# Kernel tuning notes

Hardware: AMD Instinct MI355X
Metric: run time of the kernel (lower is better)

## Reference

```python
import math
import jax, jax.numpy as jnp
import numpy as np

B, T, C, HS = 4, 4096, 1024, 64  # batch, seq, n_embd, head_size=n_embd//n_head

def setup_inputs() -> dict:
    key = jax.random.key(0)
    k0, k1, k2, k3 = jax.random.split(key, 4)
    x = jax.random.normal(k0, (B, T, C), dtype=jnp.float32)
    Wq = jax.random.normal(k1, (C, HS), dtype=jnp.float32) * 0.02
    Wk = jax.random.normal(k2, (C, HS), dtype=jnp.float32) * 0.02
    Wv = jax.random.normal(k3, (C, HS), dtype=jnp.float32) * 0.02
    return {"x": x, "Wq": Wq, "Wk": Wk, "Wv": Wv}

def reference(x, Wq, Wk, Wv):
    b, t, c = x.shape
    q = x @ Wq                                   # [B,T,hs]
    k = x @ Wk                                   # [B,T,hs]
    v = x @ Wv                                   # [B,T,hs]
    wei = jnp.einsum('btd,bsd->bts', q, k)       # [B,T,T] raw scores
    row_sums = wei.sum(axis=-1)                  # [B,T]
    k_sel = math.ceil(t / 2)                     # static: t known at trace time
    _, idx = jax.lax.top_k(row_sums, k_sel)      # [B,k_sel]
    idx = jnp.sort(idx, axis=1)
    # gather selected score rows: [B,k_sel,T]
    half_wei = jnp.take_along_axis(wei, idx[:, :, None], axis=1)
    # causal mask rows gathered from tril: tril[idx[b,i], j] == (j <= idx[b,i])
    half_mask = jnp.arange(t)[None, None, :] <= idx[:, :, None]  # [B,k_sel,T] bool
    half_wei = half_wei * (c ** -0.5)            # NOTE: scaled by n_embd, as in source
    half_wei = jnp.where(half_mask, half_wei, -jnp.inf)
    att = jax.nn.softmax(half_wei, axis=-1)      # [B,k_sel,T]
    out = att @ v                                # [B,k_sel,hs]
    return out
```

## Files before the change

### kernel.cpp

```cpp
#include <hip/hip_runtime.h>
#include <math.h>

#define BB 4
#define TT 4096
#define CC 1024
#define HS 64
#define KSEL 2048
#define NSPL 16
#define SWLOG 8
#define SW 256

typedef float f32x4 __attribute__((ext_vector_type(4)));
typedef short short8 __attribute__((ext_vector_type(8)));

__device__ __forceinline__ unsigned short f2bf(float f) {
  union { float f; unsigned int u; } c;
  c.f = f;
  const unsigned int u = c.u;
  return (unsigned short)((u + 0x7FFFu + ((u >> 16) & 1u)) >> 16);
}

__device__ __forceinline__ unsigned cvtpk(float lo, float hi) {
  unsigned r;
  asm("v_cvt_pk_bf16_f32 %0, %1, %2" : "=v"(r) : "v"(lo), "v"(hi));
  return r;
}

__global__ __launch_bounds__(256) void conv_w(const float* __restrict__ Wq,
                                              const float* __restrict__ Wk,
                                              const float* __restrict__ Wv,
                                              unsigned short* __restrict__ wbf,
                                              float* __restrict__ xsum,
                                              float* __restrict__ L,
                                              float* __restrict__ out) {
  const int gid = blockIdx.x * 256 + threadIdx.x;
  const float4 z4 = make_float4(0.f, 0.f, 0.f, 0.f);
#pragma unroll
  for (int e = 0; e < 4; e++) ((float4*)out)[gid + e * 32768] = z4;
  if (gid < 2048) ((float4*)L)[gid] = z4;
  if (gid < 1024) ((float4*)xsum)[gid] = z4;

  if (gid >= 24576) return;
  const int kt = gid / 768;
  const int rem = gid - kt * 768;
  const int nt = rem >> 6, lane = rem & 63;
  const int col = nt * 16 + (lane & 15);
  const float* W = (col < 64) ? Wq : ((col < 128) ? Wk : Wv);
  const int cl = col & 63;
  const int k0 = kt * 32 + (lane >> 4) * 8;
  unsigned short tmp[8];
#pragma unroll
  for (int i = 0; i < 8; i++) tmp[i] = f2bf(W[(size_t)(k0 + i) * HS + cl]);
  uint4 o;
  o.x = tmp[0] | ((unsigned)tmp[1] << 16);
  o.y = tmp[2] | ((unsigned)tmp[3] << 16);
  o.z = tmp[4] | ((unsigned)tmp[5] << 16);
  o.w = tmp[6] | ((unsigned)tmp[7] << 16);
  *(uint4*)(wbf + (size_t)gid * 8) = o;
}

#define PR 16
__global__ __launch_bounds__(256) void fusedproj(
    const float* __restrict__ x, const unsigned short* __restrict__ wbf,
    float* __restrict__ xsum, unsigned short* __restrict__ qbf,
    unsigned short* __restrict__ kbf, unsigned short* __restrict__ vtbf) {
  __shared__ unsigned short Xs[PR][256];
  __shared__ float xsred[4][256];
  const int rb = blockIdx.x;
  const size_t r0 = (size_t)rb * PR;
  const int tid = threadIdx.x;
  const int wid = tid >> 6, lane = tid & 63;
  const int lhi = lane >> 4, llo = lane & 15;
  const int cl = tid & 63, rg = tid >> 6;
  const int bidx = rb >> 8;

  f32x4 acc[3];
#pragma unroll
  for (int n = 0; n < 3; n++) acc[n] = (f32x4){0.f, 0.f, 0.f, 0.f};

  float4 pf[4];
#pragma unroll
  for (int rr = 0; rr < 4; rr++)
    pf[rr] = *(const float4*)(x + (r0 + rg * 4 + rr) * CC + cl * 4);

  for (int ch = 0; ch < 4; ch++) {
    float ps0 = 0.f, ps1 = 0.f, ps2 = 0.f, ps3 = 0.f;
#pragma unroll
    for (int rr = 0; rr < 4; rr++) {
      const int row = rg * 4 + rr;
      float4 v = pf[rr];
      ps0 += v.x; ps1 += v.y; ps2 += v.z; ps3 += v.w;
      *(uint2*)((char*)&Xs[0][0] + row * 512 +
                ((((cl >> 1) ^ (row & 7))) << 4) + ((cl & 1) << 3)) =
          make_uint2(cvtpk(v.x, v.y), cvtpk(v.z, v.w));
    }
    xsred[rg][cl * 4 + 0] = ps0;
    xsred[rg][cl * 4 + 1] = ps1;
    xsred[rg][cl * 4 + 2] = ps2;
    xsred[rg][cl * 4 + 3] = ps3;
    __syncthreads();
    if (ch < 3) {
#pragma unroll
      for (int rr = 0; rr < 4; rr++)
        pf[rr] = *(const float4*)(x + (r0 + rg * 4 + rr) * CC +
                                  (ch + 1) * 256 + cl * 4);
    }
    atomicAdd(&xsum[bidx * CC + ch * 256 + tid],
              xsred[0][tid] + xsred[1][tid] + xsred[2][tid] + xsred[3][tid]);
#pragma unroll
    for (int ktl = 0; ktl < 8; ktl++) {
      short8 af = *(const short8*)((const char*)&Xs[0][0] + llo * 512 +
                                   ((((ktl << 2) + lhi) ^ (llo & 7)) << 4));
      const unsigned short* bp =
          wbf + (((size_t)(ch * 8 + ktl) * 12 + wid * 3) * 64 + lane) * 8;
#pragma unroll
      for (int n = 0; n < 3; n++) {
        short8 bf = *(const short8*)(bp + n * 64 * 8);
        acc[n] = __builtin_amdgcn_mfma_f32_16x16x32_bf16(af, bf, acc[n], 0, 0, 0);
      }
    }
    __syncthreads();
  }
  const int rbg = (int)r0 + lhi * 4;
#pragma unroll
  for (int n = 0; n < 3; n++) {
    const int col = (wid * 3 + n) * 16 + llo;
    const int mat = col >> 6, cl2 = col & 63;
    if (mat == 0) {
#pragma unroll
      for (int r = 0; r < 4; r++)
        qbf[(size_t)(rbg + r) * HS + cl2] = f2bf(acc[n][r] * 0.03125f);
    } else if (mat == 1) {
#pragma unroll
      for (int r = 0; r < 4; r++)
        kbf[(size_t)(rbg + r) * HS + cl2] = f2bf(acc[n][r]);
    } else {
      const int bb = rbg >> 12, tloc = rbg & (TT - 1);
      *(uint2*)(vtbf + ((size_t)bb * HS + cl2) * TT + tloc) =
          make_uint2(cvtpk(acc[n][0], acc[n][1]), cvtpk(acc[n][2], acc[n][3]));
    }
  }
}

__global__ __launch_bounds__(512) void rowsums_x(
    const float* __restrict__ x, const float* __restrict__ Wq,
    const float* __restrict__ Wk, const float* __restrict__ xsum,
    float* __restrict__ rs) {
  __shared__ float xsl[CC];
  __shared__ float kred[8][HS];
  __shared__ float ksl[HS];
  __shared__ float wl[CC];
  const int g = blockIdx.x;
  const int tid = threadIdx.x;
  const int b = g >> 6;
  *(float2*)(xsl + tid * 2) = *(const float2*)(xsum + b * CC + tid * 2);
  __syncthreads();
  {
    const int g8 = tid >> 6, d = tid & 63;
    const float* wkp = Wk + (size_t)(g8 * 128) * HS + d;
    float s = 0.f;
    for (int c = 0; c < 128; c++) s += xsl[g8 * 128 + c] * wkp[(size_t)c * HS];
    kred[g8][d] = s;
  }
  __syncthreads();
  if (tid < 64) {
    float s = 0.f;
#pragma unroll
    for (int g8 = 0; g8 < 8; g8++) s += kred[g8][tid];
    ksl[tid] = s;
  }
  __syncthreads();
#pragma unroll
  for (int p = 0; p < 2; p++) {
    const int c = tid * 2 + p;
    const float* wqp = Wq + (size_t)c * HS;
    float s = 0.f;
#pragma unroll
    for (int d4 = 0; d4 < 16; d4++) {
      float4 a = *(const float4*)(wqp + d4 * 4);
      float4 kk = *(const float4*)(ksl + d4 * 4);
      s += a.x * kk.x + a.y * kk.y + a.z * kk.z + a.w * kk.w;
    }
    wl[c] = s;
  }
  __syncthreads();
  const size_t row = (size_t)g * 64 + (tid >> 3);
  const int qu = tid & 7;
  const float* xr = x + row * CC + qu * 128;
  const float* wr = wl + qu * 128;
  float s = 0.f;
  for (int e = 0; e < 32; e++) {
    float4 v = *(const float4*)(xr + e * 4);
    float4 w4 = *(const float4*)(wr + e * 4);
    s += v.x * w4.x + v.y * w4.y + v.z * w4.z + v.w * w4.w;
  }
  s += __shfl_xor(s, 1);
  s += __shfl_xor(s, 2);
  s += __shfl_xor(s, 4);
  if (qu == 0) rs[row] = s;
}

__global__ __launch_bounds__(256) void rankk(const float* __restrict__ rs,
                                             int* __restrict__ flag) {
  __shared__ float rl[TT];
  const int g = blockIdx.x;
  const int b = g >> 7, chunk = g & 127;
  const int tid = threadIdx.x;
  const float* rsb = rs + (size_t)b * TT;
  for (int e = tid; e < TT / 4; e += 256)
    *(float4*)(rl + e * 4) = *(const float4*)(rsb + e * 4);
  __syncthreads();
  const int cand = tid >> 3, qu = tid & 7;
  const int t = chunk * 32 + cand;
  const float my = rl[t];
  int cnt = 0;
  for (int e = 0; e < 128; e++) {
    const int s = qu * 512 + e * 4;
    float4 v = *(const float4*)(rl + s);
    cnt += (v.x > my) || (v.x == my && (s + 0) < t);
    cnt += (v.y > my) || (v.y == my && (s + 1) < t);
    cnt += (v.z > my) || (v.z == my && (s + 2) < t);
    cnt += (v.w > my) || (v.w == my && (s + 3) < t);
  }
  cnt += __shfl_xor(cnt, 1);
  cnt += __shfl_xor(cnt, 2);
  cnt += __shfl_xor(cnt, 4);
  if (qu == 0) flag[(size_t)b * TT + t] = (cnt < KSEL) ? 1 : 0;
}

__global__ __launch_bounds__(256) void compact(const int* __restrict__ flag,
                                               int* __restrict__ idx) {
  __shared__ int sums[256];
  const int b = blockIdx.x;
  const int tid = threadIdx.x;
  const int* fb = flag + (size_t)b * TT;
  const int base = tid * 16;
  int f[16];
  int cnt = 0;
#pragma unroll
  for (int e = 0; e < 16; e++) { f[e] = fb[base + e]; cnt += f[e]; }
  sums[tid] = cnt;
  __syncthreads();
  for (int d = 1; d < 256; d <<= 1) {
    int v = (tid >= d) ? sums[tid - d] : 0;
    __syncthreads();
    sums[tid] += v;
    __syncthreads();
  }
  int pos = sums[tid] - cnt;
#pragma unroll
  for (int e = 0; e < 16; e++)
    if (f[e]) idx[(size_t)b * KSEL + (pos++)] = base + e;
}

struct KF { short8 a0, a1, b0, b1; };
struct VF { short8 v0, v1, v2, v3; };

__global__ __launch_bounds__(256) void attn_mfma(
    const unsigned short* __restrict__ qbf,
    const unsigned short* __restrict__ kbf,
    const unsigned short* __restrict__ vtbf, const int* __restrict__ idx,
    float* __restrict__ L, float* __restrict__ out) {
  __shared__ unsigned short P_lds[4][32][40];
  const int rb = blockIdx.x;
  const int zz = blockIdx.y;
  const int b = blockIdx.z;
  const int tid = threadIdx.x;
  const int wid = tid >> 6, lane = tid & 63;
  const int s = zz * 4 + wid;
  const size_t rbase = (size_t)b * KSEL + rb * 32;
  const int tmaxblk = idx[rbase + 31];
  const int jlo = s << SWLOG;
  if (jlo > tmaxblk) return;

  const int lhi = lane >> 4, llo = lane & 15;
  const int trow0 = idx[rbase + llo];
  const int trow1 = idx[rbase + 16 + llo];
  short8 qf[2][2];
  {
    const unsigned short* qp0 = qbf + ((size_t)b * TT + trow0) * HS + lhi * 8;
    const unsigned short* qp1 = qbf + ((size_t)b * TT + trow1) * HS + lhi * 8;
    qf[0][0] = *(const short8*)(qp0);
    qf[0][1] = *(const short8*)(qp0 + 32);
    qf[1][0] = *(const short8*)(qp1);
    qf[1][1] = *(const short8*)(qp1 + 32);
  }
  f32x4 o[2][4];
#pragma unroll
  for (int mtt = 0; mtt < 2; mtt++)
#pragma unroll
    for (int n = 0; n < 4; n++) o[mtt][n] = (f32x4){0.f, 0.f, 0.f, 0.f};
  float lsum[2] = {0.f, 0.f};

  const unsigned short* kb = kbf + (size_t)b * TT * HS;
  const unsigned short* vb = vtbf + (size_t)b * HS * TT;
  const int jend = min(tmaxblk + 1, jlo + SW);

  auto loadK = [&](int j0) {
    KF K;
    const unsigned short* kp = kb + (size_t)(j0 + llo) * HS + lhi * 8;
    K.a0 = *(const short8*)(kp);
    K.a1 = *(const short8*)(kp + 32);
    K.b0 = *(const short8*)(kp + 16 * HS);
    K.b1 = *(const short8*)(kp + 16 * HS + 32);
    return K;
  };
  auto loadV = [&](int j0) {
    VF V;
    const unsigned short* vp = vb + (size_t)llo * TT + j0 + lhi * 8;
    V.v0 = *(const short8*)(vp);
    V.v1 = *(const short8*)(vp + 16 * TT);
    V.v2 = *(const short8*)(vp + 32 * TT);
    V.v3 = *(const short8*)(vp + 48 * TT);
    return V;
  };

  auto body = [&](int j0, const KF& K, const VF& V) {
    f32x4 sc[2][2];
#pragma unroll
    for (int mtt = 0; mtt < 2; mtt++) {
      f32x4 a = (f32x4){0.f, 0.f, 0.f, 0.f};
      a = __builtin_amdgcn_mfma_f32_16x16x32_bf16(K.a0, qf[mtt][0], a, 0, 0, 0);
      a = __builtin_amdgcn_mfma_f32_16x16x32_bf16(K.a1, qf[mtt][1], a, 0, 0, 0);
      sc[mtt][0] = a;
      f32x4 c = (f32x4){0.f, 0.f, 0.f, 0.f};
      c = __builtin_amdgcn_mfma_f32_16x16x32_bf16(K.b0, qf[mtt][0], c, 0, 0, 0);
      c = __builtin_amdgcn_mfma_f32_16x16x32_bf16(K.b1, qf[mtt][1], c, 0, 0, 0);
      sc[mtt][1] = c;
    }
#pragma unroll
    for (int mtt = 0; mtt < 2; mtt++) {
      const int tr = (mtt == 0) ? trow0 : trow1;
      float p[8];
#pragma unroll
      for (int kt = 0; kt < 2; kt++)
#pragma unroll
        for (int r = 0; r < 4; r++) {
          const int kk = j0 + kt * 16 + lhi * 4 + r;
          const float e = __expf(sc[mtt][kt][r]);
          p[kt * 4 + r] = (kk <= tr) ? e : 0.f;
        }
      lsum[mtt] += ((p[0] + p[1]) + (p[2] + p[3])) +
                   ((p[4] + p[5]) + (p[6] + p[7]));
      *(uint2*)&P_lds[wid][mtt * 16 + llo][lhi * 4] =
          make_uint2(cvtpk(p[0], p[1]), cvtpk(p[2], p[3]));
      *(uint2*)&P_lds[wid][mtt * 16 + llo][16 + lhi * 4] =
          make_uint2(cvtpk(p[4], p[5]), cvtpk(p[6], p[7]));
    }
    short8 pa0 = *(const short8*)&P_lds[wid][llo][lhi * 8];
    short8 pa1 = *(const short8*)&P_lds[wid][16 + llo][lhi * 8];
    o[0][0] = __builtin_amdgcn_mfma_f32_16x16x32_bf16(pa0, V.v0, o[0][0], 0, 0, 0);
    o[1][0] = __builtin_amdgcn_mfma_f32_16x16x32_bf16(pa1, V.v0, o[1][0], 0, 0, 0);
    o[0][1] = __builtin_amdgcn_mfma_f32_16x16x32_bf16(pa0, V.v1, o[0][1], 0, 0, 0);
    o[1][1] = __builtin_amdgcn_mfma_f32_16x16x32_bf16(pa1, V.v1, o[1][1], 0, 0, 0);
    o[0][2] = __builtin_amdgcn_mfma_f32_16x16x32_bf16(pa0, V.v2, o[0][2], 0, 0, 0);
    o[1][2] = __builtin_amdgcn_mfma_f32_16x16x32_bf16(pa1, V.v2, o[1][2], 0, 0, 0);
    o[0][3] = __builtin_amdgcn_mfma_f32_16x16x32_bf16(pa0, V.v3, o[0][3], 0, 0, 0);
    o[1][3] = __builtin_amdgcn_mfma_f32_16x16x32_bf16(pa1, V.v3, o[1][3], 0, 0, 0);
  };

  int j0 = jlo;
  KF ka = loadK(j0), kb2;
  VF va = loadV(j0), vb2;
  for (;;) {
    if (j0 + 32 < jend) { kb2 = loadK(j0 + 32); vb2 = loadV(j0 + 32); }
    body(j0, ka, va);
    j0 += 32;
    if (j0 >= jend) break;
    if (j0 + 32 < jend) { ka = loadK(j0 + 32); va = loadV(j0 + 32); }
    body(j0, kb2, vb2);
    j0 += 32;
    if (j0 >= jend) break;
  }

  lsum[0] += __shfl_xor(lsum[0], 16);
  lsum[0] += __shfl_xor(lsum[0], 32);
  lsum[1] += __shfl_xor(lsum[1], 16);
  lsum[1] += __shfl_xor(lsum[1], 32);
  if (lane < 16) {
    atomicAdd(&L[rbase + llo], lsum[0]);
    atomicAdd(&L[rbase + 16 + llo], lsum[1]);
  }
#pragma unroll
  for (int mtt = 0; mtt < 2; mtt++)
#pragma unroll
    for (int r = 0; r < 4; r++) {
      float* op = out + (rbase + mtt * 16 + lhi * 4 + r) * HS;
#pragma unroll
      for (int n = 0; n < 4; n++) atomicAdd(op + n * 16 + llo, o[mtt][n][r]);
    }
}

__global__ __launch_bounds__(256) void normalize(const float* __restrict__ L,
                                                 float* __restrict__ out) {
  const int gid = blockIdx.x * 256 + threadIdx.x;
  const float invl = 1.0f / L[gid >> 4];
  float4 v = ((float4*)out)[gid];
  v.x *= invl; v.y *= invl; v.z *= invl; v.w *= invl;
  ((float4*)out)[gid] = v;
}

extern "C" void kernel_launch(void* const* d_in, const int* in_sizes, int n_in,
                              void* d_out, int out_size, void* d_ws,
                              size_t ws_size, hipStream_t stream) {
  const float* x = (const float*)d_in[0];
  const float* Wq = (const float*)d_in[1];
  const float* Wk = (const float*)d_in[2];
  const float* Wv = (const float*)d_in[3];
  float* out = (float*)d_out;

  float* wsf = (float*)d_ws;
  float* xsum = wsf;
  float* rs = xsum + 4096;
  int* flag = (int*)(rs + 16384);
  float* L = (float*)(flag + 16384);
  unsigned short* wbf = (unsigned short*)(L + 8192);
  unsigned short* qbf = wbf + 196608;
  unsigned short* kbf = qbf + 1048576;
  unsigned short* vtbf = kbf + 1048576;
  int* idxp = (int*)(vtbf + 1048576);

  conv_w<<<128, 256, 0, stream>>>(Wq, Wk, Wv, wbf, xsum, L, out);
  fusedproj<<<1024, 256, 0, stream>>>(x, wbf, xsum, qbf, kbf, vtbf);
  rowsums_x<<<256, 512, 0, stream>>>(x, Wq, Wk, xsum, rs);
  rankk<<<512, 256, 0, stream>>>(rs, flag);
  compact<<<BB, 256, 0, stream>>>(flag, idxp);
  attn_mfma<<<dim3(64, 4, BB), 256, 0, stream>>>(qbf, kbf, vtbf, idxp, L, out);
  normalize<<<512, 256, 0, stream>>>(L, out);
}
```

Measured before the change: 134.3 us.

## Fuse rank and compact via last-block pattern; replace attention atomics with split reduction

The rank kernel and the compaction kernel are merged. The last block to finish for each batch, found through an atomic counter, does the prefix-sum compaction, now with a wave-shuffle scan instead of a shared-memory Hillis-Steele scan. The attention kernel no longer atomically adds partial outputs and row sums into zeroed buffers. Each split writes its partial into a workspace, and the last-arriving wave per row block reduces and normalizes, which removes the zero-fill of the output and the separate normalize launch. The trade-offs are extra workspace traffic, a serial 32-row reduction tail in one wave, and a partial-sum buffer that reuses workspace memory already consumed by earlier stages.

```diff
diff --git a/kernel.cpp b/kernel.cpp
--- a/kernel.cpp
+++ b/kernel.cpp
@@ -31,16 +31,10 @@
                                               const float* __restrict__ Wv,
                                               unsigned short* __restrict__ wbf,
                                               float* __restrict__ xsum,
-                                              float* __restrict__ L,
-                                              float* __restrict__ out) {
+                                              int* __restrict__ cnts) {
   const int gid = blockIdx.x * 256 + threadIdx.x;
-  const float4 z4 = make_float4(0.f, 0.f, 0.f, 0.f);
-#pragma unroll
-  for (int e = 0; e < 4; e++) ((float4*)out)[gid + e * 32768] = z4;
-  if (gid < 2048) ((float4*)L)[gid] = z4;
-  if (gid < 1024) ((float4*)xsum)[gid] = z4;
-
-  if (gid >= 24576) return;
+  if (gid < 1024) ((float4*)xsum)[gid] = make_float4(0.f, 0.f, 0.f, 0.f);
+  if (gid < 66) ((int4*)cnts)[gid] = make_int4(0, 0, 0, 0);
   const int kt = gid / 768;
   const int rem = gid - kt * 768;
   const int nt = rem >> 6, lane = rem & 63;
@@ -200,57 +194,74 @@
   if (qu == 0) rs[row] = s;
 }
 
-__global__ __launch_bounds__(256) void rankk(const float* __restrict__ rs,
-                                             int* __restrict__ flag) {
+__global__ __launch_bounds__(256) void rankk_compact(
+    const float* __restrict__ rs, int* __restrict__ flag,
+    int* __restrict__ idxp, int* __restrict__ cnt_rk) {
   __shared__ float rl[TT];
+  __shared__ int lastFlag;
   const int g = blockIdx.x;
   const int b = g >> 7, chunk = g & 127;
   const int tid = threadIdx.x;
+  const int wid = tid >> 6, lane = tid & 63;
   const float* rsb = rs + (size_t)b * TT;
   for (int e = tid; e < TT / 4; e += 256)
     *(float4*)(rl + e * 4) = *(const float4*)(rsb + e * 4);
   __syncthreads();
-  const int cand = tid >> 3, qu = tid & 7;
-  const int t = chunk * 32 + cand;
-  const float my = rl[t];
-  int cnt = 0;
-  for (int e = 0; e < 128; e++) {
-    const int s = qu * 512 + e * 4;
-    float4 v = *(const float4*)(rl + s);
-    cnt += (v.x > my) || (v.x == my && (s + 0) < t);
-    cnt += (v.y > my) || (v.y == my && (s + 1) < t);
-    cnt += (v.z > my) || (v.z == my && (s + 2) < t);
-    cnt += (v.w > my) || (v.w == my && (s + 3) < t);
-  }
-  cnt += __shfl_xor(cnt, 1);
-  cnt += __shfl_xor(cnt, 2);
-  cnt += __shfl_xor(cnt, 4);
-  if (qu == 0) flag[(size_t)b * TT + t] = (cnt < KSEL) ? 1 : 0;
-}
-
-__global__ __launch_bounds__(256) void compact(const int* __restrict__ flag,
-                                               int* __restrict__ idx) {
-  __shared__ int sums[256];
-  const int b = blockIdx.x;
-  const int tid = threadIdx.x;
+  {
+    const int cand = tid >> 3, qu = tid & 7;
+    const int t = chunk * 32 + cand;
+    const float my = rl[t];
+    int cnt = 0;
+    for (int e = 0; e < 128; e++) {
+      const int s = qu * 512 + e * 4;
+      float4 v = *(const float4*)(rl + s);
+      cnt += (v.x > my) || (v.x == my && (s + 0) < t);
+      cnt += (v.y > my) || (v.y == my && (s + 1) < t);
+      cnt += (v.z > my) || (v.z == my && (s + 2) < t);
+      cnt += (v.w > my) || (v.w == my && (s + 3) < t);
+    }
+    cnt += __shfl_xor(cnt, 1);
+    cnt += __shfl_xor(cnt, 2);
+    cnt += __shfl_xor(cnt, 4);
+    if (qu == 0) flag[(size_t)b * TT + t] = (cnt < KSEL) ? 1 : 0;
+  }
+  __threadfence();
+  __syncthreads();
+  if (tid == 0) lastFlag = (atomicAdd(&cnt_rk[b], 1) == 127);
+  __syncthreads();
+  if (!lastFlag) return;
+  __threadfence();
+  __shared__ int wsum[4];
+  __shared__ int woff[4];
   const int* fb = flag + (size_t)b * TT;
   const int base = tid * 16;
   int f[16];
   int cnt = 0;
 #pragma unroll
-  for (int e = 0; e < 16; e++) { f[e] = fb[base + e]; cnt += f[e]; }
-  sums[tid] = cnt;
-  __syncthreads();
-  for (int d = 1; d < 256; d <<= 1) {
-    int v = (tid >= d) ? sums[tid - d] : 0;
-    __syncthreads();
-    sums[tid] += v;
-    __syncthreads();
-  }
-  int pos = sums[tid] - cnt;
+  for (int e4 = 0; e4 < 4; e4++) {
+    int4 v = *(const int4*)(fb + base + e4 * 4);
+    f[e4 * 4 + 0] = v.x; f[e4 * 4 + 1] = v.y;
+    f[e4 * 4 + 2] = v.z; f[e4 * 4 + 3] = v.w;
+    cnt += v.x + v.y + v.z + v.w;
+  }
+  int sc = cnt;
+#pragma unroll
+  for (int d = 1; d < 64; d <<= 1) {
+    int v = __shfl_up(sc, d);
+    if (lane >= d) sc += v;
+  }
+  if (lane == 63) wsum[wid] = sc;
+  __syncthreads();
+  if (tid == 0) {
+    int a = 0;
+#pragma unroll
+    for (int w = 0; w < 4; w++) { woff[w] = a; a += wsum[w]; }
+  }
+  __syncthreads();
+  int pos = woff[wid] + sc - cnt;
 #pragma unroll
   for (int e = 0; e < 16; e++)
-    if (f[e]) idx[(size_t)b * KSEL + (pos++)] = base + e;
+    if (f[e]) idxp[(size_t)b * KSEL + (pos++)] = base + e;
 }
 
 struct KF { short8 a0, a1, b0, b1; };
@@ -260,7 +271,8 @@
     const unsigned short* __restrict__ qbf,
     const unsigned short* __restrict__ kbf,
     const unsigned short* __restrict__ vtbf, const int* __restrict__ idx,
-    float* __restrict__ L, float* __restrict__ out) {
+    float* __restrict__ pl, float* __restrict__ pacc,
+    int* __restrict__ cnt_at, float* __restrict__ out) {
   __shared__ unsigned short P_lds[4][32][40];
   const int rb = blockIdx.x;
   const int zz = blockIdx.y;
@@ -378,26 +390,38 @@
   lsum[1] += __shfl_xor(lsum[1], 16);
   lsum[1] += __shfl_xor(lsum[1], 32);
   if (lane < 16) {
-    atomicAdd(&L[rbase + llo], lsum[0]);
-    atomicAdd(&L[rbase + 16 + llo], lsum[1]);
+    pl[(rbase + llo) * NSPL + s] = lsum[0];
+    pl[(rbase + 16 + llo) * NSPL + s] = lsum[1];
   }
 #pragma unroll
   for (int mtt = 0; mtt < 2; mtt++)
 #pragma unroll
     for (int r = 0; r < 4; r++) {
-      float* op = out + (rbase + mtt * 16 + lhi * 4 + r) * HS;
-#pragma unroll
-      for (int n = 0; n < 4; n++) atomicAdd(op + n * 16 + llo, o[mtt][n][r]);
-    }
-}
-
-__global__ __launch_bounds__(256) void normalize(const float* __restrict__ L,
-                                                 float* __restrict__ out) {
-  const int gid = blockIdx.x * 256 + threadIdx.x;
-  const float invl = 1.0f / L[gid >> 4];
-  float4 v = ((float4*)out)[gid];
-  v.x *= invl; v.y *= invl; v.z *= invl; v.w *= invl;
-  ((float4*)out)[gid] = v;
+      const size_t rowi = rbase + mtt * 16 + lhi * 4 + r;
+#pragma unroll
+      for (int n = 0; n < 4; n++)
+        pacc[(rowi * NSPL + s) * HS + n * 16 + llo] = o[mtt][n][r];
+    }
+
+  __threadfence();
+  int old = 0;
+  if (lane == 0) old = atomicAdd(&cnt_at[b * 64 + rb], 1);
+  old = __shfl(old, 0);
+  const int nact = (tmaxblk >> SWLOG) + 1;
+  if (old != nact - 1) return;
+  __threadfence();
+#pragma unroll 1
+  for (int r = 0; r < 32; ++r) {
+    const size_t rowi = rbase + r;
+    const int nsr = (idx[rowi] >> SWLOG) + 1;
+    float L = 0.f;
+    float osum = 0.f;
+    for (int ss = 0; ss < nsr; ++ss) {
+      L += pl[rowi * NSPL + ss];
+      osum += pacc[(rowi * NSPL + ss) * HS + lane];
+    }
+    out[rowi * HS + lane] = osum / L;
+  }
 }
 
 extern "C" void kernel_launch(void* const* d_in, const int* in_sizes, int n_in,
@@ -410,21 +434,24 @@
   float* out = (float*)d_out;
 
   float* wsf = (float*)d_ws;
+  float* pacc = wsf;
   float* xsum = wsf;
   float* rs = xsum + 4096;
   int* flag = (int*)(rs + 16384);
-  float* L = (float*)(flag + 16384);
-  unsigned short* wbf = (unsigned short*)(L + 8192);
-  unsigned short* qbf = wbf + 196608;
+  unsigned short* wbf = (unsigned short*)(flag + 16384);
+  unsigned short* qbf = (unsigned short*)(pacc + 8388608);
   unsigned short* kbf = qbf + 1048576;
   unsigned short* vtbf = kbf + 1048576;
   int* idxp = (int*)(vtbf + 1048576);
-
-  conv_w<<<128, 256, 0, stream>>>(Wq, Wk, Wv, wbf, xsum, L, out);
+  float* pl = (float*)(idxp + 8192);
+  int* cnts = (int*)(pl + 131072);
+  int* cnt_rk = cnts;
+  int* cnt_at = cnts + 8;
+
+  conv_w<<<96, 256, 0, stream>>>(Wq, Wk, Wv, wbf, xsum, cnts);
   fusedproj<<<1024, 256, 0, stream>>>(x, wbf, xsum, qbf, kbf, vtbf);
   rowsums_x<<<256, 512, 0, stream>>>(x, Wq, Wk, xsum, rs);
-  rankk<<<512, 256, 0, stream>>>(rs, flag);
-  compact<<<BB, 256, 0, stream>>>(flag, idxp);
-  attn_mfma<<<dim3(64, 4, BB), 256, 0, stream>>>(qbf, kbf, vtbf, idxp, L, out);
-  normalize<<<512, 256, 0, stream>>>(L, out);
-}
+  rankk_compact<<<512, 256, 0, stream>>>(rs, flag, idxp, cnt_rk);
+  attn_mfma<<<dim3(64, 4, BB), 256, 0, stream>>>(qbf, kbf, vtbf, idxp, pl,
+                                                 pacc, cnt_at, out);
+}
```

Result: slower. 365.7 us (+172.3%).
